# Performance work log

Measured on AMD Instinct MI355X. Metric: run time of the kernel, lower is better.

The kernel has to match this reference:

```python
import jax, jax.numpy as jnp
from jax import lax
import numpy as np

B, T, H, I, O = 256, 2048, 150, 1, 1

def setup_inputs() -> dict:
    key = jax.random.key(0)
    ks = jax.random.split(key, 7)
    s = 1.0 / np.sqrt(H)
    return {
        "input": jax.random.normal(ks[0], (B, T), dtype=jnp.float32),
        "W_ih": jax.random.uniform(ks[1], (3 * H, I), jnp.float32, -s, s),
        "W_hh": jax.random.uniform(ks[2], (3 * H, H), jnp.float32, -s, s),
        "b_ih": jax.random.uniform(ks[3], (3 * H,), jnp.float32, -s, s),
        "b_hh": jax.random.uniform(ks[4], (3 * H,), jnp.float32, -s, s),
        "W_lin": jax.random.uniform(ks[5], (O, H), jnp.float32, -s, s),
        "b_lin": jax.random.uniform(ks[6], (O,), jnp.float32, -s, s),
    }

def reference(input, W_ih, W_hh, b_ih, b_hh, W_lin, b_lin):
    # input: [B, T]; GRUCell recurrence with relu on hidden, per-step linear head.
    hidden = W_hh.shape[1]

    def step(h, x_t):  # h: [B, H], x_t: [B, 1]
        gi = x_t @ W_ih.T + b_ih          # [B, 3H]
        gh = h @ W_hh.T + b_hh            # [B, 3H]
        i_r, i_z, i_n = jnp.split(gi, 3, axis=-1)
        h_r, h_z, h_n = jnp.split(gh, 3, axis=-1)
        r = jax.nn.sigmoid(i_r + h_r)
        z = jax.nn.sigmoid(i_z + h_z)
        n = jnp.tanh(i_n + r * h_n)
        h_new = jax.nn.relu((1.0 - z) * n + z * h)  # relu applied as in original
        y = h_new @ W_lin.T + b_lin       # [B, 1]
        return h_new, y

    xs = jnp.transpose(input)[:, :, None]            # [T, B, 1]
    h0 = jnp.zeros((input.shape[0], hidden), input.dtype)
    _, ys = lax.scan(step, h0, xs)                   # ys: [T, B, 1]
    return jnp.transpose(ys[:, :, 0])                # [B, T] (stack dim=1, squeeze(2))
```

## Files before the change

### kernel.cpp

```cpp
#include <hip/hip_runtime.h>
#include <math.h>


#define BB 256
#define TT 2048
#define HH 150
#define H3 450

typedef float fx2 __attribute__((ext_vector_type(2)));

#define WCLOB \
  "v100","v101","v102","v103","v104","v105","v106","v107","v108","v109", \
  "v110","v111","v112","v113","v114","v115","v116","v117","v118","v119", \
  "v120","v121","v122","v123","v124","v125","v126","v127","v128","v129", \
  "v130","v131","v132","v133","v134","v135","v136","v137","v138","v139", \
  "v140","v141","v142","v143","v144","v145","v146","v147","v148","v149", \
  "v150","v151","v152","v153","v154","v155","v156","v157","v158","v159", \
  "v160","v161","v162","v163","v164","v165","v166","v167","v168","v169", \
  "v170","v171","v172","v173","v174","v175","v176","v177","v178","v179", \
  "v180","v181","v182","v183","v184","v185","v186","v187","v188","v189", \
  "v190","v191","v192","v193","v194","v195","v196","v197","v198","v199", \
  "v200","v201","v202","v203","v204","v205","v206","v207","v208","v209", \
  "v210","v211","v212","v213","v214","v215","v216","v217","v218","v219", \
  "v220","v221","v222","v223","v224","v225","v226","v227","v228","v229", \
  "v230","v231","v232","v233","v234","v235","v236","v237","v238","v239", \
  "v240","v241","v242","v243","v244","v245","v246","v247","v248","v249", \
  "v250","v251"

#define LD4(vA0,vA1,vB0,vB1,OFF) \
  "global_load_dword v" #vA0 ", %[b0], off offset:" #OFF "\n\t" \
  "global_load_dword v" #vA1 ", %[b1], off offset:" #OFF "\n\t" \
  "global_load_dword v" #vB0 ", %[b2], off offset:" #OFF "\n\t" \
  "global_load_dword v" #vB1 ", %[b3], off offset:" #OFF "\n\t"

#define PKB(sp, vp, acc) \
  "v_pk_fma_f32 " acc ", " sp ", " vp ", " acc " op_sel:[0,0,0] op_sel_hi:[0,1,1]\n\t"

#define G4(m0,m1,m2,m3, A0,B0, A1,B1, A2,B2, A3,B3) \
  "v_readlane_b32 s20, %[hq], " #m0 "\n\t" \
  "v_readlane_b32 s22, %[hq], " #m1 "\n\t" \
  "v_readlane_b32 s24, %[hq], " #m2 "\n\t" \
  "v_readlane_b32 s26, %[hq], " #m3 "\n\t" \
  PKB("s[20:21]", A0, "%[a01]") PKB("s[20:21]", B0, "%[a23]") \
  PKB("s[22:23]", A1, "%[a01]") PKB("s[22:23]", B1, "%[a23]") \
  PKB("s[24:25]", A2, "%[a01]") PKB("s[24:25]", B2, "%[a23]") \
  PKB("s[26:27]", A3, "%[a01]") PKB("s[26:27]", B3, "%[a23]")

__global__ __launch_bounds__(512, 2) void gru_seq_kernel(
    const float* __restrict__ input,
    const float* __restrict__ W_ih,
    const float* __restrict__ W_hh,
    const float* __restrict__ b_ih,
    const float* __restrict__ b_hh,
    const float* __restrict__ W_lin,
    const float* __restrict__ b_lin,
    float* __restrict__ out)
{
    const int b    = blockIdx.x;
    const int tid  = threadIdx.x;
    const int lane = tid & 63;
    const int wid  = tid >> 6;
    const int q    = wid & 3;
    const int idx  = ((wid >> 2) << 6) + lane;

    __shared__ float  xrow[TT];
    __shared__ float4 h4[64];
    __shared__ float  PPf[2048];
    __shared__ float  yout[TT];

    ((float4*)xrow)[tid] = ((const float4*)(input + (size_t)b * TT))[tid];
    if (tid < 64) h4[tid] = make_float4(0.f, 0.f, 0.f, 0.f);

    const int r0 = 4 * idx;
#define ROWP(r) ((r) == H3 ? W_lin : W_hh + ((r) < H3 ? (r) : (H3 - 1)) * HH)
    const float* b0 = ROWP(r0)     + q;
    const float* b1 = ROWP(r0 + 1) + q;
    const float* b2 = ROWP(r0 + 2) + q;
    const float* b3 = ROWP(r0 + 3) + q;

    asm volatile(
        LD4(100,101,176,177,0)    LD4(102,103,178,179,16)
        LD4(104,105,180,181,32)   LD4(106,107,182,183,48)
        LD4(108,109,184,185,64)   LD4(110,111,186,187,80)
        LD4(112,113,188,189,96)   LD4(114,115,190,191,112)
        LD4(116,117,192,193,128)  LD4(118,119,194,195,144)
        LD4(120,121,196,197,160)  LD4(122,123,198,199,176)
        LD4(124,125,200,201,192)  LD4(126,127,202,203,208)
        LD4(128,129,204,205,224)  LD4(130,131,206,207,240)
        LD4(132,133,208,209,256)  LD4(134,135,210,211,272)
        LD4(136,137,212,213,288)  LD4(138,139,214,215,304)
        LD4(140,141,216,217,320)  LD4(142,143,218,219,336)
        LD4(144,145,220,221,352)  LD4(146,147,222,223,368)
        LD4(148,149,224,225,384)  LD4(150,151,226,227,400)
        LD4(152,153,228,229,416)  LD4(154,155,230,231,432)
        LD4(156,157,232,233,448)  LD4(158,159,234,235,464)
        LD4(160,161,236,237,480)  LD4(162,163,238,239,496)
        LD4(164,165,240,241,512)  LD4(166,167,242,243,528)
        LD4(168,169,244,245,544)  LD4(170,171,246,247,560)
        LD4(172,173,248,249,576)
        "s_waitcnt vmcnt(0)\n\t"
        :
        : [b0] "v"(b0), [b1] "v"(b1), [b2] "v"(b2), [b3] "v"(b3)
        : WCLOB, "memory");
    {
        const int t37 = (q < 2) ? 148 : 144;
        float w0 = b0[t37], w1 = b1[t37], w2 = b2[t37], w3 = b3[t37];
        asm volatile(
            "v_mov_b32 v174, %0\n\tv_mov_b32 v175, %1\n\t"
            "v_mov_b32 v250, %2\n\tv_mov_b32 v251, %3\n\t"
            :: "v"(w0), "v"(w1), "v"(w2), "v"(w3)
            : "v174","v175","v250","v251");
    }

    float wih_r = 0.f, wih_z = 0.f, wih_n = 0.f;
    float bih_r = 0.f, bih_z = 0.f, bih_n = 0.f;
    float bhh_r = 0.f, bhh_z = 0.f, bhh_n = 0.f;
    if (tid < HH) {
        wih_r = W_ih[tid];          bih_r = b_ih[tid];          bhh_r = b_hh[tid];
        wih_z = W_ih[HH + tid];     bih_z = b_ih[HH + tid];     bhh_z = b_hh[HH + tid];
        wih_n = W_ih[2 * HH + tid]; bih_n = b_ih[2 * HH + tid]; bhh_n = b_hh[2 * HH + tid];
    }
    const float blin = b_lin[0];
    float hreg = 0.f;
    float* outb = out + (size_t)b * TT;
    float2* st01 = (float2*)PPf          + (q << 7) + idx;
    float2* st23 = (float2*)(PPf + 1024) + (q << 7) + idx;
    int ir = 0, iz = 0, in_ = 0;
    if (tid < HH) {
        int r;
        r = tid;        ir  = (((r & 3) >> 1) << 10) + ((r >> 2) << 1) + (r & 1);
        r = HH + tid;   iz  = (((r & 3) >> 1) << 10) + ((r >> 2) << 1) + (r & 1);
        r = 2*HH + tid; in_ = (((r & 3) >> 1) << 10) + ((r >> 2) << 1) + (r & 1);
    }
    const int iy = 1024 + (112 << 1);

    __syncthreads();

    for (int t = 0; t <= TT; ++t) {
        float4 hv = h4[lane];
        float hq = (q == 0) ? hv.x : (q == 1) ? hv.y : (q == 2) ? hv.z : hv.w;
        fx2 a01; a01.x = 0.f; a01.y = 0.f;
        fx2 a23; a23.x = 0.f; a23.y = 0.f;
        asm volatile(
            G4( 0, 1, 2, 3, "v[100:101]","v[176:177]", "v[102:103]","v[178:179]",
                            "v[104:105]","v[180:181]", "v[106:107]","v[182:183]")
            G4( 4, 5, 6, 7, "v[108:109]","v[184:185]", "v[110:111]","v[186:187]",
                            "v[112:113]","v[188:189]", "v[114:115]","v[190:191]")
            G4( 8, 9,10,11, "v[116:117]","v[192:193]", "v[118:119]","v[194:195]",
                            "v[120:121]","v[196:197]", "v[122:123]","v[198:199]")
            G4(12,13,14,15, "v[124:125]","v[200:201]", "v[126:127]","v[202:203]",
                            "v[128:129]","v[204:205]", "v[130:131]","v[206:207]")
            G4(16,17,18,19, "v[132:133]","v[208:209]", "v[134:135]","v[210:211]",
                            "v[136:137]","v[212:213]", "v[138:139]","v[214:215]")
            G4(20,21,22,23, "v[140:141]","v[216:217]", "v[142:143]","v[218:219]",
                            "v[144:145]","v[220:221]", "v[146:147]","v[222:223]")
            G4(24,25,26,27, "v[148:149]","v[224:225]", "v[150:151]","v[226:227]",
                            "v[152:153]","v[228:229]", "v[154:155]","v[230:231]")
            G4(28,29,30,31, "v[156:157]","v[232:233]", "v[158:159]","v[234:235]",
                            "v[160:161]","v[236:237]", "v[162:163]","v[238:239]")
            "v_readlane_b32 s20, %[hq], 32\n\t"
            "v_readlane_b32 s22, %[hq], 33\n\t"
            "v_readlane_b32 s24, %[hq], 34\n\t"
            "v_readlane_b32 s26, %[hq], 35\n\t"
            "v_readlane_b32 s28, %[hq], 36\n\t"
            "v_readlane_b32 s30, %[hq], 37\n\t"
            PKB("s[20:21]", "v[164:165]", "%[a01]")
            PKB("s[20:21]", "v[240:241]", "%[a23]")
            PKB("s[22:23]", "v[166:167]", "%[a01]")
            PKB("s[22:23]", "v[242:243]", "%[a23]")
            PKB("s[24:25]", "v[168:169]", "%[a01]")
            PKB("s[24:25]", "v[244:245]", "%[a23]")
            PKB("s[26:27]", "v[170:171]", "%[a01]")
            PKB("s[26:27]", "v[246:247]", "%[a23]")
            PKB("s[28:29]", "v[172:173]", "%[a01]")
            PKB("s[28:29]", "v[248:249]", "%[a23]")
            PKB("s[30:31]", "v[174:175]", "%[a01]")
            PKB("s[30:31]", "v[250:251]", "%[a23]")
            : [a01] "+v"(a01), [a23] "+v"(a23)
            : [hq] "v"(hq)
            : "s20","s22","s24","s26","s28","s30", WCLOB);
        float2 s0; s0.x = a01.x; s0.y = a01.y;
        float2 s1; s1.x = a23.x; s1.y = a23.y;
        *st01 = s0;
        *st23 = s1;
        __syncthreads();

        if (t < TT && tid < HH) {
            float x  = xrow[t];
            float pr = ((PPf[ir]        + PPf[ir + 256])
                      + (PPf[ir + 512]  + PPf[ir + 768]))  + bhh_r;
            float pz = ((PPf[iz]        + PPf[iz + 256])
                      + (PPf[iz + 512]  + PPf[iz + 768]))  + bhh_z;
            float pn = ((PPf[in_]       + PPf[in_ + 256])
                      + (PPf[in_ + 512] + PPf[in_ + 768])) + bhh_n;
            float gr = fmaf(x, wih_r, bih_r) + pr;
            float gz = fmaf(x, wih_z, bih_z) + pz;
            float r  = 1.f / (1.f + __expf(-gr));
            float z  = 1.f / (1.f + __expf(-gz));
            float ta = fmaf(x, wih_n, bih_n) + r * pn;
            ta = fminf(fmaxf(ta, -15.f), 15.f);
            float e  = __expf(2.f * ta);
            float n  = (e - 1.f) / (e + 1.f);
            float hnew = fmaf(z, hreg - n, n);
            hnew = fmaxf(hnew, 0.f);
            hreg = hnew;
            ((float*)h4)[tid] = hnew;
        }
        if (t > 0 && tid == H3) {
            yout[t - 1] = ((PPf[iy]       + PPf[iy + 256])
                         + (PPf[iy + 512] + PPf[iy + 768])) + blin;
        }
        __syncthreads();
    }

    ((float4*)outb)[tid] = ((const float4*)yout)[tid];
}

extern "C" void kernel_launch(void* const* d_in, const int* in_sizes, int n_in,
                              void* d_out, int out_size, void* d_ws, size_t ws_size,
                              hipStream_t stream) {
    const float* input = (const float*)d_in[0];
    const float* W_ih  = (const float*)d_in[1];
    const float* W_hh  = (const float*)d_in[2];
    const float* b_ih  = (const float*)d_in[3];
    const float* b_hh  = (const float*)d_in[4];
    const float* W_lin = (const float*)d_in[5];
    const float* b_lin = (const float*)d_in[6];
    float* out = (float*)d_out;

    gru_seq_kernel<<<dim3(BB), dim3(512), 0, stream>>>(
        input, W_ih, W_hh, b_ih, b_hh, W_lin, b_lin, out);
}
```

Baseline: 1.834 ms.

## Double-buffer partial sums and keep hidden state in the consuming lanes

Double-buffers the shared partial-sum array so each time step needs only one barrier instead of two. The gate work is remapped so that lane u = 4*lane+q of every wave computes exactly the hidden unit that lane later broadcasts via readlane. This removes the shared h4 round trip, and the unit is computed redundantly in each wave. The output-head reduction is folded into one lane of wave 0. The trade-off is redundant transcendental work in all 8 waves and extra register pressure, with correctness resting on the lane mapping and the parity of the buffers.

```diff
diff --git a/kernel.cpp b/kernel.cpp
--- a/kernel.cpp
+++ b/kernel.cpp
@@ -63,13 +63,11 @@
     const int q    = wid & 3;
     const int idx  = ((wid >> 2) << 6) + lane;
 
-    __shared__ float  xrow[TT];
-    __shared__ float4 h4[64];
-    __shared__ float  PPf[2048];
-    __shared__ float  yout[TT];
+    __shared__ float xrow[TT];
+    __shared__ float PPf[2][2048];
+    __shared__ float yout[TT];
 
     ((float4*)xrow)[tid] = ((const float4*)(input + (size_t)b * TT))[tid];
-    if (tid < 64) h4[tid] = make_float4(0.f, 0.f, 0.f, 0.f);
 
     const int r0 = 4 * idx;
 #define ROWP(r) ((r) == H3 ? W_lin : W_hh + ((r) < H3 ? (r) : (H3 - 1)) * HH)
@@ -112,33 +110,40 @@
             : "v174","v175","v250","v251");
     }
 
+    const int  u       = 4 * lane + q;
+    const bool valid   = (lane < 38) && (u < HH);
+    const bool ywriter = (wid == 0) && (lane == 38);
     float wih_r = 0.f, wih_z = 0.f, wih_n = 0.f;
     float bih_r = 0.f, bih_z = 0.f, bih_n = 0.f;
     float bhh_r = 0.f, bhh_z = 0.f, bhh_n = 0.f;
-    if (tid < HH) {
-        wih_r = W_ih[tid];          bih_r = b_ih[tid];          bhh_r = b_hh[tid];
-        wih_z = W_ih[HH + tid];     bih_z = b_ih[HH + tid];     bhh_z = b_hh[HH + tid];
-        wih_n = W_ih[2 * HH + tid]; bih_n = b_ih[2 * HH + tid]; bhh_n = b_hh[2 * HH + tid];
-    }
-    const float blin = b_lin[0];
-    float hreg = 0.f;
+    if (valid) {
+        wih_r = W_ih[u];          bih_r = b_ih[u];          bhh_r = b_hh[u];
+        wih_z = W_ih[HH + u];     bih_z = b_ih[HH + u];     bhh_z = b_hh[HH + u];
+        wih_n = W_ih[2 * HH + u]; bih_n = b_ih[2 * HH + u]; bhh_n = b_hh[2 * HH + u];
+    }
+    int ir = 0, iz = 0, in_ = 0;
+    if (valid) {
+        int r;
+        r = u;          ir  = (((r & 3) >> 1) << 10) + ((r >> 2) << 1) + (r & 1);
+        r = HH + u;     iz  = (((r & 3) >> 1) << 10) + ((r >> 2) << 1) + (r & 1);
+        r = 2*HH + u;   in_ = (((r & 3) >> 1) << 10) + ((r >> 2) << 1) + (r & 1);
+    }
+    if (ywriter) {
+        ir    = 1024 + (112 << 1);
+        bhh_r = b_lin[0];
+    }
+
+    float hq = 0.f;
     float* outb = out + (size_t)b * TT;
-    float2* st01 = (float2*)PPf          + (q << 7) + idx;
-    float2* st23 = (float2*)(PPf + 1024) + (q << 7) + idx;
-    int ir = 0, iz = 0, in_ = 0;
-    if (tid < HH) {
-        int r;
-        r = tid;        ir  = (((r & 3) >> 1) << 10) + ((r >> 2) << 1) + (r & 1);
-        r = HH + tid;   iz  = (((r & 3) >> 1) << 10) + ((r >> 2) << 1) + (r & 1);
-        r = 2*HH + tid; in_ = (((r & 3) >> 1) << 10) + ((r >> 2) << 1) + (r & 1);
-    }
-    const int iy = 1024 + (112 << 1);
+    float2* st01 = (float2*)PPf + (q << 7) + idx;
+    float2* st23 = (float2*)PPf + 512 + (q << 7) + idx;
 
     __syncthreads();
 
     for (int t = 0; t <= TT; ++t) {
-        float4 hv = h4[lane];
-        float hq = (q == 0) ? hv.x : (q == 1) ? hv.y : (q == 2) ? hv.z : hv.w;
+        const int sel = t & 1;
+        float xt = xrow[t & (TT - 1)];
+
         fx2 a01; a01.x = 0.f; a01.y = 0.f;
         fx2 a23; a23.x = 0.f; a23.y = 0.f;
         asm volatile(
@@ -181,38 +186,36 @@
             : "s20","s22","s24","s26","s28","s30", WCLOB);
         float2 s0; s0.x = a01.x; s0.y = a01.y;
         float2 s1; s1.x = a23.x; s1.y = a23.y;
-        *st01 = s0;
-        *st23 = s1;
+        *(st01 + (sel << 10)) = s0;
+        *(st23 + (sel << 10)) = s1;
         __syncthreads();
 
-        if (t < TT && tid < HH) {
-            float x  = xrow[t];
-            float pr = ((PPf[ir]        + PPf[ir + 256])
-                      + (PPf[ir + 512]  + PPf[ir + 768]))  + bhh_r;
-            float pz = ((PPf[iz]        + PPf[iz + 256])
-                      + (PPf[iz + 512]  + PPf[iz + 768]))  + bhh_z;
-            float pn = ((PPf[in_]       + PPf[in_ + 256])
-                      + (PPf[in_ + 512] + PPf[in_ + 768])) + bhh_n;
-            float gr = fmaf(x, wih_r, bih_r) + pr;
-            float gz = fmaf(x, wih_z, bih_z) + pz;
-            float r  = 1.f / (1.f + __expf(-gr));
-            float z  = 1.f / (1.f + __expf(-gz));
-            float ta = fmaf(x, wih_n, bih_n) + r * pn;
-            ta = fminf(fmaxf(ta, -15.f), 15.f);
-            float e  = __expf(2.f * ta);
-            float n  = (e - 1.f) / (e + 1.f);
-            float hnew = fmaf(z, hreg - n, n);
-            hnew = fmaxf(hnew, 0.f);
-            hreg = hnew;
-            ((float*)h4)[tid] = hnew;
+        const float* pb = &PPf[0][0] + (sel << 11);
+        if ((valid && t < TT) || ywriter) {
+            float pr = ((pb[ir]        + pb[ir + 256])
+                      + (pb[ir + 512]  + pb[ir + 768]))  + bhh_r;
+            if (ywriter) {
+                if (t > 0) yout[t - 1] = pr;
+            } else {
+                float pz = ((pb[iz]        + pb[iz + 256])
+                          + (pb[iz + 512]  + pb[iz + 768]))  + bhh_z;
+                float pn = ((pb[in_]       + pb[in_ + 256])
+                          + (pb[in_ + 512] + pb[in_ + 768])) + bhh_n;
+                float gr = fmaf(xt, wih_r, bih_r) + pr;
+                float gz = fmaf(xt, wih_z, bih_z) + pz;
+                float rr = 1.f / (1.f + __expf(-gr));
+                float zz = 1.f / (1.f + __expf(-gz));
+                float ta = fmaf(xt, wih_n, bih_n) + rr * pn;
+                ta = fminf(fmaxf(ta, -15.f), 15.f);
+                float e  = __expf(2.f * ta);
+                float nn = (e - 1.f) / (e + 1.f);
+                float hnew = fmaf(zz, hq - nn, nn);
+                hq = fmaxf(hnew, 0.f);
+            }
         }
-        if (t > 0 && tid == H3) {
-            yout[t - 1] = ((PPf[iy]       + PPf[iy + 256])
-                         + (PPf[iy + 512] + PPf[iy + 768])) + blin;
-        }
-        __syncthreads();
-    }
-
+    }
+
+    __syncthreads();
     ((float4*)outb)[tid] = ((const float4*)yout)[tid];
 }
 
```

After: 1.991 ms. 1.09x slower.

## Repartition GRU matvec: 8 rows per lane, K split across 8 waves

Applied to the files above, without the earlier changes.

Reorganizes the per-step hidden matvec so each lane owns 8 output rows and each of the 8 waves handles a stride-8 slice of the hidden dimension, replacing 4 rows per lane with a 4-way K split. The goal is to shorten each wave's serial FMA/readlane chain per time step (19 K elements instead of 38), which is the critical path of the recurrence. In exchange, the cross-wave reduction grows from 4 to 8 partial sums per gate, adding LDS reads in the gate-update phase. The LDS layout is padded (stride 65/520) to avoid bank conflicts.

```diff
diff --git a/kernel.cpp b/kernel.cpp
--- a/kernel.cpp
+++ b/kernel.cpp
@@ -27,24 +27,32 @@
   "v240","v241","v242","v243","v244","v245","v246","v247","v248","v249", \
   "v250","v251"
 
-#define LD4(vA0,vA1,vB0,vB1,OFF) \
-  "global_load_dword v" #vA0 ", %[b0], off offset:" #OFF "\n\t" \
-  "global_load_dword v" #vA1 ", %[b1], off offset:" #OFF "\n\t" \
-  "global_load_dword v" #vB0 ", %[b2], off offset:" #OFF "\n\t" \
-  "global_load_dword v" #vB1 ", %[b3], off offset:" #OFF "\n\t"
+#define LD8(a0,a1,b0,b1,c0,c1,d0,d1,OFF) \
+  "global_load_dword v" #a0 ", %[p0], off offset:" #OFF "\n\t" \
+  "global_load_dword v" #a1 ", %[p1], off offset:" #OFF "\n\t" \
+  "global_load_dword v" #b0 ", %[p2], off offset:" #OFF "\n\t" \
+  "global_load_dword v" #b1 ", %[p3], off offset:" #OFF "\n\t" \
+  "global_load_dword v" #c0 ", %[p4], off offset:" #OFF "\n\t" \
+  "global_load_dword v" #c1 ", %[p5], off offset:" #OFF "\n\t" \
+  "global_load_dword v" #d0 ", %[p6], off offset:" #OFF "\n\t" \
+  "global_load_dword v" #d1 ", %[p7], off offset:" #OFF "\n\t"
 
 #define PKB(sp, vp, acc) \
   "v_pk_fma_f32 " acc ", " sp ", " vp ", " acc " op_sel:[0,0,0] op_sel_hi:[0,1,1]\n\t"
 
-#define G4(m0,m1,m2,m3, A0,B0, A1,B1, A2,B2, A3,B3) \
+#define G4(m0,m1,m2,m3, A0,B0,C0,D0, A1,B1,C1,D1, A2,B2,C2,D2, A3,B3,C3,D3) \
   "v_readlane_b32 s20, %[hq], " #m0 "\n\t" \
   "v_readlane_b32 s22, %[hq], " #m1 "\n\t" \
   "v_readlane_b32 s24, %[hq], " #m2 "\n\t" \
   "v_readlane_b32 s26, %[hq], " #m3 "\n\t" \
   PKB("s[20:21]", A0, "%[a01]") PKB("s[20:21]", B0, "%[a23]") \
+  PKB("s[20:21]", C0, "%[a45]") PKB("s[20:21]", D0, "%[a67]") \
   PKB("s[22:23]", A1, "%[a01]") PKB("s[22:23]", B1, "%[a23]") \
+  PKB("s[22:23]", C1, "%[a45]") PKB("s[22:23]", D1, "%[a67]") \
   PKB("s[24:25]", A2, "%[a01]") PKB("s[24:25]", B2, "%[a23]") \
-  PKB("s[26:27]", A3, "%[a01]") PKB("s[26:27]", B3, "%[a23]")
+  PKB("s[24:25]", C2, "%[a45]") PKB("s[24:25]", D2, "%[a67]") \
+  PKB("s[26:27]", A3, "%[a01]") PKB("s[26:27]", B3, "%[a23]") \
+  PKB("s[26:27]", C3, "%[a45]") PKB("s[26:27]", D3, "%[a67]")
 
 __global__ __launch_bounds__(512, 2) void gru_seq_kernel(
     const float* __restrict__ input,
@@ -60,56 +68,63 @@
     const int tid  = threadIdx.x;
     const int lane = tid & 63;
     const int wid  = tid >> 6;
-    const int q    = wid & 3;
-    const int idx  = ((wid >> 2) << 6) + lane;
-
-    __shared__ float  xrow[TT];
-    __shared__ float4 h4[64];
-    __shared__ float  PPf[2048];
-    __shared__ float  yout[TT];
+
+    __shared__ float xrow[TT];
+    __shared__ float PPf[4160];
+    __shared__ float hb[520];
+    __shared__ float yout[TT];
 
     ((float4*)xrow)[tid] = ((const float4*)(input + (size_t)b * TT))[tid];
-    if (tid < 64) h4[tid] = make_float4(0.f, 0.f, 0.f, 0.f);
-
-    const int r0 = 4 * idx;
+    hb[tid < 512 ? tid : 0] = 0.f;
+    if (tid < 8) hb[512 + tid] = 0.f;
+
+    const int r0 = 8 * lane;
 #define ROWP(r) ((r) == H3 ? W_lin : W_hh + ((r) < H3 ? (r) : (H3 - 1)) * HH)
-    const float* b0 = ROWP(r0)     + q;
-    const float* b1 = ROWP(r0 + 1) + q;
-    const float* b2 = ROWP(r0 + 2) + q;
-    const float* b3 = ROWP(r0 + 3) + q;
+    const float* p0 = ROWP(r0)     + wid;
+    const float* p1 = ROWP(r0 + 1) + wid;
+    const float* p2 = ROWP(r0 + 2) + wid;
+    const float* p3 = ROWP(r0 + 3) + wid;
+    const float* p4 = ROWP(r0 + 4) + wid;
+    const float* p5 = ROWP(r0 + 5) + wid;
+    const float* p6 = ROWP(r0 + 6) + wid;
+    const float* p7 = ROWP(r0 + 7) + wid;
 
     asm volatile(
-        LD4(100,101,176,177,0)    LD4(102,103,178,179,16)
-        LD4(104,105,180,181,32)   LD4(106,107,182,183,48)
-        LD4(108,109,184,185,64)   LD4(110,111,186,187,80)
-        LD4(112,113,188,189,96)   LD4(114,115,190,191,112)
-        LD4(116,117,192,193,128)  LD4(118,119,194,195,144)
-        LD4(120,121,196,197,160)  LD4(122,123,198,199,176)
-        LD4(124,125,200,201,192)  LD4(126,127,202,203,208)
-        LD4(128,129,204,205,224)  LD4(130,131,206,207,240)
-        LD4(132,133,208,209,256)  LD4(134,135,210,211,272)
-        LD4(136,137,212,213,288)  LD4(138,139,214,215,304)
-        LD4(140,141,216,217,320)  LD4(142,143,218,219,336)
-        LD4(144,145,220,221,352)  LD4(146,147,222,223,368)
-        LD4(148,149,224,225,384)  LD4(150,151,226,227,400)
-        LD4(152,153,228,229,416)  LD4(154,155,230,231,432)
-        LD4(156,157,232,233,448)  LD4(158,159,234,235,464)
-        LD4(160,161,236,237,480)  LD4(162,163,238,239,496)
-        LD4(164,165,240,241,512)  LD4(166,167,242,243,528)
-        LD4(168,169,244,245,544)  LD4(170,171,246,247,560)
-        LD4(172,173,248,249,576)
+        LD8(100,101,138,139,176,177,214,215, 0)
+        LD8(102,103,140,141,178,179,216,217, 32)
+        LD8(104,105,142,143,180,181,218,219, 64)
+        LD8(106,107,144,145,182,183,220,221, 96)
+        LD8(108,109,146,147,184,185,222,223, 128)
+        LD8(110,111,148,149,186,187,224,225, 160)
+        LD8(112,113,150,151,188,189,226,227, 192)
+        LD8(114,115,152,153,190,191,228,229, 224)
+        LD8(116,117,154,155,192,193,230,231, 256)
+        LD8(118,119,156,157,194,195,232,233, 288)
+        LD8(120,121,158,159,196,197,234,235, 320)
+        LD8(122,123,160,161,198,199,236,237, 352)
+        LD8(124,125,162,163,200,201,238,239, 384)
+        LD8(126,127,164,165,202,203,240,241, 416)
+        LD8(128,129,166,167,204,205,242,243, 448)
+        LD8(130,131,168,169,206,207,244,245, 480)
+        LD8(132,133,170,171,208,209,246,247, 512)
+        LD8(134,135,172,173,210,211,248,249, 544)
         "s_waitcnt vmcnt(0)\n\t"
         :
-        : [b0] "v"(b0), [b1] "v"(b1), [b2] "v"(b2), [b3] "v"(b3)
+        : [p0] "v"(p0), [p1] "v"(p1), [p2] "v"(p2), [p3] "v"(p3),
+          [p4] "v"(p4), [p5] "v"(p5), [p6] "v"(p6), [p7] "v"(p7)
         : WCLOB, "memory");
     {
-        const int t37 = (q < 2) ? 148 : 144;
-        float w0 = b0[t37], w1 = b1[t37], w2 = b2[t37], w3 = b3[t37];
+        const int t18 = (wid < 6) ? 144 : 136;
+        float w0 = p0[t18], w1 = p1[t18], w2 = p2[t18], w3 = p3[t18];
+        float w4 = p4[t18], w5 = p5[t18], w6 = p6[t18], w7 = p7[t18];
         asm volatile(
-            "v_mov_b32 v174, %0\n\tv_mov_b32 v175, %1\n\t"
-            "v_mov_b32 v250, %2\n\tv_mov_b32 v251, %3\n\t"
-            :: "v"(w0), "v"(w1), "v"(w2), "v"(w3)
-            : "v174","v175","v250","v251");
+            "v_mov_b32 v136, %0\n\tv_mov_b32 v137, %1\n\t"
+            "v_mov_b32 v174, %2\n\tv_mov_b32 v175, %3\n\t"
+            "v_mov_b32 v212, %4\n\tv_mov_b32 v213, %5\n\t"
+            "v_mov_b32 v250, %6\n\tv_mov_b32 v251, %7\n\t"
+            :: "v"(w0), "v"(w1), "v"(w2), "v"(w3),
+               "v"(w4), "v"(w5), "v"(w6), "v"(w7)
+            : "v136","v137","v174","v175","v212","v213","v250","v251");
     }
 
     float wih_r = 0.f, wih_z = 0.f, wih_n = 0.f;
@@ -123,76 +138,88 @@
     const float blin = b_lin[0];
     float hreg = 0.f;
     float* outb = out + (size_t)b * TT;
-    float2* st01 = (float2*)PPf          + (q << 7) + idx;
-    float2* st23 = (float2*)(PPf + 1024) + (q << 7) + idx;
+    float2* st = (float2*)PPf + wid * 260 + lane;
     int ir = 0, iz = 0, in_ = 0;
     if (tid < HH) {
         int r;
-        r = tid;        ir  = (((r & 3) >> 1) << 10) + ((r >> 2) << 1) + (r & 1);
-        r = HH + tid;   iz  = (((r & 3) >> 1) << 10) + ((r >> 2) << 1) + (r & 1);
-        r = 2*HH + tid; in_ = (((r & 3) >> 1) << 10) + ((r >> 2) << 1) + (r & 1);
-    }
-    const int iy = 1024 + (112 << 1);
+        r = tid;        ir  = (((r & 7) >> 1) * 65 + (r >> 3)) * 2 + (r & 1);
+        r = HH + tid;   iz  = (((r & 7) >> 1) * 65 + (r >> 3)) * 2 + (r & 1);
+        r = 2*HH + tid; in_ = (((r & 7) >> 1) * 65 + (r >> 3)) * 2 + (r & 1);
+    }
+    const int iy = (1 * 65 + 56) * 2;
 
     __syncthreads();
 
     for (int t = 0; t <= TT; ++t) {
-        float4 hv = h4[lane];
-        float hq = (q == 0) ? hv.x : (q == 1) ? hv.y : (q == 2) ? hv.z : hv.w;
+        float hq = hb[wid * 65 + lane];
         fx2 a01; a01.x = 0.f; a01.y = 0.f;
         fx2 a23; a23.x = 0.f; a23.y = 0.f;
+        fx2 a45; a45.x = 0.f; a45.y = 0.f;
+        fx2 a67; a67.x = 0.f; a67.y = 0.f;
         asm volatile(
-            G4( 0, 1, 2, 3, "v[100:101]","v[176:177]", "v[102:103]","v[178:179]",
-                            "v[104:105]","v[180:181]", "v[106:107]","v[182:183]")
-            G4( 4, 5, 6, 7, "v[108:109]","v[184:185]", "v[110:111]","v[186:187]",
-                            "v[112:113]","v[188:189]", "v[114:115]","v[190:191]")
-            G4( 8, 9,10,11, "v[116:117]","v[192:193]", "v[118:119]","v[194:195]",
-                            "v[120:121]","v[196:197]", "v[122:123]","v[198:199]")
-            G4(12,13,14,15, "v[124:125]","v[200:201]", "v[126:127]","v[202:203]",
-                            "v[128:129]","v[204:205]", "v[130:131]","v[206:207]")
-            G4(16,17,18,19, "v[132:133]","v[208:209]", "v[134:135]","v[210:211]",
-                            "v[136:137]","v[212:213]", "v[138:139]","v[214:215]")
-            G4(20,21,22,23, "v[140:141]","v[216:217]", "v[142:143]","v[218:219]",
-                            "v[144:145]","v[220:221]", "v[146:147]","v[222:223]")
-            G4(24,25,26,27, "v[148:149]","v[224:225]", "v[150:151]","v[226:227]",
-                            "v[152:153]","v[228:229]", "v[154:155]","v[230:231]")
-            G4(28,29,30,31, "v[156:157]","v[232:233]", "v[158:159]","v[234:235]",
-                            "v[160:161]","v[236:237]", "v[162:163]","v[238:239]")
-            "v_readlane_b32 s20, %[hq], 32\n\t"
-            "v_readlane_b32 s22, %[hq], 33\n\t"
-            "v_readlane_b32 s24, %[hq], 34\n\t"
-            "v_readlane_b32 s26, %[hq], 35\n\t"
-            "v_readlane_b32 s28, %[hq], 36\n\t"
-            "v_readlane_b32 s30, %[hq], 37\n\t"
-            PKB("s[20:21]", "v[164:165]", "%[a01]")
-            PKB("s[20:21]", "v[240:241]", "%[a23]")
-            PKB("s[22:23]", "v[166:167]", "%[a01]")
-            PKB("s[22:23]", "v[242:243]", "%[a23]")
-            PKB("s[24:25]", "v[168:169]", "%[a01]")
-            PKB("s[24:25]", "v[244:245]", "%[a23]")
-            PKB("s[26:27]", "v[170:171]", "%[a01]")
-            PKB("s[26:27]", "v[246:247]", "%[a23]")
-            PKB("s[28:29]", "v[172:173]", "%[a01]")
-            PKB("s[28:29]", "v[248:249]", "%[a23]")
-            PKB("s[30:31]", "v[174:175]", "%[a01]")
-            PKB("s[30:31]", "v[250:251]", "%[a23]")
-            : [a01] "+v"(a01), [a23] "+v"(a23)
+            G4( 0, 1, 2, 3,
+                "v[100:101]","v[138:139]","v[176:177]","v[214:215]",
+                "v[102:103]","v[140:141]","v[178:179]","v[216:217]",
+                "v[104:105]","v[142:143]","v[180:181]","v[218:219]",
+                "v[106:107]","v[144:145]","v[182:183]","v[220:221]")
+            G4( 4, 5, 6, 7,
+                "v[108:109]","v[146:147]","v[184:185]","v[222:223]",
+                "v[110:111]","v[148:149]","v[186:187]","v[224:225]",
+                "v[112:113]","v[150:151]","v[188:189]","v[226:227]",
+                "v[114:115]","v[152:153]","v[190:191]","v[228:229]")
+            G4( 8, 9,10,11,
+                "v[116:117]","v[154:155]","v[192:193]","v[230:231]",
+                "v[118:119]","v[156:157]","v[194:195]","v[232:233]",
+                "v[120:121]","v[158:159]","v[196:197]","v[234:235]",
+                "v[122:123]","v[160:161]","v[198:199]","v[236:237]")
+            G4(12,13,14,15,
+                "v[124:125]","v[162:163]","v[200:201]","v[238:239]",
+                "v[126:127]","v[164:165]","v[202:203]","v[240:241]",
+                "v[128:129]","v[166:167]","v[204:205]","v[242:243]",
+                "v[130:131]","v[168:169]","v[206:207]","v[244:245]")
+            "v_readlane_b32 s28, %[hq], 16\n\t"
+            "v_readlane_b32 s30, %[hq], 17\n\t"
+            "v_readlane_b32 s20, %[hq], 18\n\t"
+            PKB("s[28:29]", "v[132:133]", "%[a01]")
+            PKB("s[28:29]", "v[170:171]", "%[a23]")
+            PKB("s[28:29]", "v[208:209]", "%[a45]")
+            PKB("s[28:29]", "v[246:247]", "%[a67]")
+            PKB("s[30:31]", "v[134:135]", "%[a01]")
+            PKB("s[30:31]", "v[172:173]", "%[a23]")
+            PKB("s[30:31]", "v[210:211]", "%[a45]")
+            PKB("s[30:31]", "v[248:249]", "%[a67]")
+            PKB("s[20:21]", "v[136:137]", "%[a01]")
+            PKB("s[20:21]", "v[174:175]", "%[a23]")
+            PKB("s[20:21]", "v[212:213]", "%[a45]")
+            PKB("s[20:21]", "v[250:251]", "%[a67]")
+            : [a01] "+v"(a01), [a23] "+v"(a23),
+              [a45] "+v"(a45), [a67] "+v"(a67)
             : [hq] "v"(hq)
             : "s20","s22","s24","s26","s28","s30", WCLOB);
-        float2 s0; s0.x = a01.x; s0.y = a01.y;
-        float2 s1; s1.x = a23.x; s1.y = a23.y;
-        *st01 = s0;
-        *st23 = s1;
+        float2 s01; s01.x = a01.x; s01.y = a01.y;
+        float2 s23; s23.x = a23.x; s23.y = a23.y;
+        float2 s45; s45.x = a45.x; s45.y = a45.y;
+        float2 s67; s67.x = a67.x; s67.y = a67.y;
+        st[0]   = s01;
+        st[65]  = s23;
+        st[130] = s45;
+        st[195] = s67;
         __syncthreads();
 
         if (t < TT && tid < HH) {
             float x  = xrow[t];
-            float pr = ((PPf[ir]        + PPf[ir + 256])
-                      + (PPf[ir + 512]  + PPf[ir + 768]))  + bhh_r;
-            float pz = ((PPf[iz]        + PPf[iz + 256])
-                      + (PPf[iz + 512]  + PPf[iz + 768]))  + bhh_z;
-            float pn = ((PPf[in_]       + PPf[in_ + 256])
-                      + (PPf[in_ + 512] + PPf[in_ + 768])) + bhh_n;
+            float pr = (((PPf[ir]         + PPf[ir + 520])
+                       + (PPf[ir + 1040]  + PPf[ir + 1560]))
+                      + ((PPf[ir + 2080]  + PPf[ir + 2600])
+                       + (PPf[ir + 3120]  + PPf[ir + 3640]))) + bhh_r;
+            float pz = (((PPf[iz]         + PPf[iz + 520])
+                       + (PPf[iz + 1040]  + PPf[iz + 1560]))
+                      + ((PPf[iz + 2080]  + PPf[iz + 2600])
+                       + (PPf[iz + 3120]  + PPf[iz + 3640]))) + bhh_z;
+            float pn = (((PPf[in_]        + PPf[in_ + 520])
+                       + (PPf[in_ + 1040] + PPf[in_ + 1560]))
+                      + ((PPf[in_ + 2080] + PPf[in_ + 2600])
+                       + (PPf[in_ + 3120] + PPf[in_ + 3640]))) + bhh_n;
             float gr = fmaf(x, wih_r, bih_r) + pr;
             float gz = fmaf(x, wih_z, bih_z) + pz;
             float r  = 1.f / (1.f + __expf(-gr));
@@ -204,11 +231,13 @@
             float hnew = fmaf(z, hreg - n, n);
             hnew = fmaxf(hnew, 0.f);
             hreg = hnew;
-            ((float*)h4)[tid] = hnew;
+            hb[(tid & 7) * 65 + (tid >> 3)] = hnew;
         }
         if (t > 0 && tid == H3) {
-            yout[t - 1] = ((PPf[iy]       + PPf[iy + 256])
-                         + (PPf[iy + 512] + PPf[iy + 768])) + blin;
+            yout[t - 1] = (((PPf[iy]        + PPf[iy + 520])
+                          + (PPf[iy + 1040] + PPf[iy + 1560]))
+                         + ((PPf[iy + 2080] + PPf[iy + 2600])
+                          + (PPf[iy + 3120] + PPf[iy + 3640]))) + blin;
         }
         __syncthreads();
     }
```

Result: slower. 1.881 ms (+2.6%).

## Broadcast hidden state via LDS reads instead of readlane, pad partial-sum buffer

Applied to the files above, without the earlier changes.

Replaces the per-step v_readlane scalar broadcast of the hidden vector with ds_read_b64 loads from a transposed shared hidden buffer, feeding packed FMAs through op_sel halves and pipelining the LDS reads against compute with staged waitcnts. The partial-sum buffer is padded (strides 130/260/520) to reduce bank conflicts, and the divisions in sigmoid/tanh become hardware reciprocal approximations. The goal is to remove the serial readlane/SGPR dependency chain and bank conflicts in the recurrence's critical path. It risks LDS latency exposure and slightly less accurate activations.

```diff
diff --git a/kernel.cpp b/kernel.cpp
--- a/kernel.cpp
+++ b/kernel.cpp
@@ -27,24 +27,26 @@
   "v240","v241","v242","v243","v244","v245","v246","v247","v248","v249", \
   "v250","v251"
 
+#define HCLOB \
+  "v80","v81","v82","v83","v84","v85","v86","v87","v88","v89", \
+  "v90","v91","v92","v93","v94","v95","v96","v97","v98","v99"
+
 #define LD4(vA0,vA1,vB0,vB1,OFF) \
   "global_load_dword v" #vA0 ", %[b0], off offset:" #OFF "\n\t" \
   "global_load_dword v" #vA1 ", %[b1], off offset:" #OFF "\n\t" \
   "global_load_dword v" #vB0 ", %[b2], off offset:" #OFF "\n\t" \
   "global_load_dword v" #vB1 ", %[b3], off offset:" #OFF "\n\t"
 
-#define PKB(sp, vp, acc) \
-  "v_pk_fma_f32 " acc ", " sp ", " vp ", " acc " op_sel:[0,0,0] op_sel_hi:[0,1,1]\n\t"
-
-#define G4(m0,m1,m2,m3, A0,B0, A1,B1, A2,B2, A3,B3) \
-  "v_readlane_b32 s20, %[hq], " #m0 "\n\t" \
-  "v_readlane_b32 s22, %[hq], " #m1 "\n\t" \
-  "v_readlane_b32 s24, %[hq], " #m2 "\n\t" \
-  "v_readlane_b32 s26, %[hq], " #m3 "\n\t" \
-  PKB("s[20:21]", A0, "%[a01]") PKB("s[20:21]", B0, "%[a23]") \
-  PKB("s[22:23]", A1, "%[a01]") PKB("s[22:23]", B1, "%[a23]") \
-  PKB("s[24:25]", A2, "%[a01]") PKB("s[24:25]", B2, "%[a23]") \
-  PKB("s[26:27]", A3, "%[a01]") PKB("s[26:27]", B3, "%[a23]")
+#define PKBL(hp, wp, acc) \
+  "v_pk_fma_f32 " acc ", " hp ", " wp ", " acc " op_sel:[0,0,0] op_sel_hi:[0,1,1]\n\t"
+#define PKBH(hp, wp, acc) \
+  "v_pk_fma_f32 " acc ", " hp ", " wp ", " acc " op_sel:[1,0,0] op_sel_hi:[1,1,1]\n\t"
+#define PKML(hp, wp, acc) \
+  "v_pk_mul_f32 " acc ", " hp ", " wp " op_sel:[0,0] op_sel_hi:[0,1]\n\t"
+
+#define C0(P, A, B)  PKML(P, A, "%[a01]") PKML(P, B, "%[a23]")
+#define CPL(P, A, B) PKBL(P, A, "%[a01]") PKBL(P, B, "%[a23]")
+#define CPH(P, A, B) PKBH(P, A, "%[a01]") PKBH(P, B, "%[a23]")
 
 __global__ __launch_bounds__(512, 2) void gru_seq_kernel(
     const float* __restrict__ input,
@@ -63,13 +65,13 @@
     const int q    = wid & 3;
     const int idx  = ((wid >> 2) << 6) + lane;
 
-    __shared__ float  xrow[TT];
-    __shared__ float4 h4[64];
-    __shared__ float  PPf[2048];
-    __shared__ float  yout[TT];
+    __shared__ float xrow[TT];
+    __shared__ float PPf[2080];
+    __shared__ __align__(16) float hb[160];
+    __shared__ float yout[TT];
 
     ((float4*)xrow)[tid] = ((const float4*)(input + (size_t)b * TT))[tid];
-    if (tid < 64) h4[tid] = make_float4(0.f, 0.f, 0.f, 0.f);
+    if (tid < 160) hb[tid] = 0.f;
 
     const int r0 = 4 * idx;
 #define ROWP(r) ((r) == H3 ? W_lin : W_hh + ((r) < H3 ? (r) : (H3 - 1)) * HH)
@@ -123,92 +125,122 @@
     const float blin = b_lin[0];
     float hreg = 0.f;
     float* outb = out + (size_t)b * TT;
-    float2* st01 = (float2*)PPf          + (q << 7) + idx;
-    float2* st23 = (float2*)(PPf + 1024) + (q << 7) + idx;
+    float2* st = (float2*)PPf + q * 130 + idx;
+    const unsigned hva = (unsigned)(size_t)(&hb[q * 40]);
     int ir = 0, iz = 0, in_ = 0;
     if (tid < HH) {
         int r;
-        r = tid;        ir  = (((r & 3) >> 1) << 10) + ((r >> 2) << 1) + (r & 1);
-        r = HH + tid;   iz  = (((r & 3) >> 1) << 10) + ((r >> 2) << 1) + (r & 1);
-        r = 2*HH + tid; in_ = (((r & 3) >> 1) << 10) + ((r >> 2) << 1) + (r & 1);
-    }
-    const int iy = 1024 + (112 << 1);
+        r = tid;        ir  = ((r & 3) >> 1) * 1040 + ((r >> 2) << 1) + (r & 1);
+        r = HH + tid;   iz  = ((r & 3) >> 1) * 1040 + ((r >> 2) << 1) + (r & 1);
+        r = 2*HH + tid; in_ = ((r & 3) >> 1) * 1040 + ((r >> 2) << 1) + (r & 1);
+    }
+    const int iy = 1040 + 112 * 2;
 
     __syncthreads();
 
     for (int t = 0; t <= TT; ++t) {
-        float4 hv = h4[lane];
-        float hq = (q == 0) ? hv.x : (q == 1) ? hv.y : (q == 2) ? hv.z : hv.w;
-        fx2 a01; a01.x = 0.f; a01.y = 0.f;
-        fx2 a23; a23.x = 0.f; a23.y = 0.f;
+        fx2 a01, a23;
         asm volatile(
-            G4( 0, 1, 2, 3, "v[100:101]","v[176:177]", "v[102:103]","v[178:179]",
-                            "v[104:105]","v[180:181]", "v[106:107]","v[182:183]")
-            G4( 4, 5, 6, 7, "v[108:109]","v[184:185]", "v[110:111]","v[186:187]",
-                            "v[112:113]","v[188:189]", "v[114:115]","v[190:191]")
-            G4( 8, 9,10,11, "v[116:117]","v[192:193]", "v[118:119]","v[194:195]",
-                            "v[120:121]","v[196:197]", "v[122:123]","v[198:199]")
-            G4(12,13,14,15, "v[124:125]","v[200:201]", "v[126:127]","v[202:203]",
-                            "v[128:129]","v[204:205]", "v[130:131]","v[206:207]")
-            G4(16,17,18,19, "v[132:133]","v[208:209]", "v[134:135]","v[210:211]",
-                            "v[136:137]","v[212:213]", "v[138:139]","v[214:215]")
-            G4(20,21,22,23, "v[140:141]","v[216:217]", "v[142:143]","v[218:219]",
-                            "v[144:145]","v[220:221]", "v[146:147]","v[222:223]")
-            G4(24,25,26,27, "v[148:149]","v[224:225]", "v[150:151]","v[226:227]",
-                            "v[152:153]","v[228:229]", "v[154:155]","v[230:231]")
-            G4(28,29,30,31, "v[156:157]","v[232:233]", "v[158:159]","v[234:235]",
-                            "v[160:161]","v[236:237]", "v[162:163]","v[238:239]")
-            "v_readlane_b32 s20, %[hq], 32\n\t"
-            "v_readlane_b32 s22, %[hq], 33\n\t"
-            "v_readlane_b32 s24, %[hq], 34\n\t"
-            "v_readlane_b32 s26, %[hq], 35\n\t"
-            "v_readlane_b32 s28, %[hq], 36\n\t"
-            "v_readlane_b32 s30, %[hq], 37\n\t"
-            PKB("s[20:21]", "v[164:165]", "%[a01]")
-            PKB("s[20:21]", "v[240:241]", "%[a23]")
-            PKB("s[22:23]", "v[166:167]", "%[a01]")
-            PKB("s[22:23]", "v[242:243]", "%[a23]")
-            PKB("s[24:25]", "v[168:169]", "%[a01]")
-            PKB("s[24:25]", "v[244:245]", "%[a23]")
-            PKB("s[26:27]", "v[170:171]", "%[a01]")
-            PKB("s[26:27]", "v[246:247]", "%[a23]")
-            PKB("s[28:29]", "v[172:173]", "%[a01]")
-            PKB("s[28:29]", "v[248:249]", "%[a23]")
-            PKB("s[30:31]", "v[174:175]", "%[a01]")
-            PKB("s[30:31]", "v[250:251]", "%[a23]")
-            : [a01] "+v"(a01), [a23] "+v"(a23)
-            : [hq] "v"(hq)
-            : "s20","s22","s24","s26","s28","s30", WCLOB);
-        float2 s0; s0.x = a01.x; s0.y = a01.y;
-        float2 s1; s1.x = a23.x; s1.y = a23.y;
-        *st01 = s0;
-        *st23 = s1;
+            "ds_read_b64 v[80:81], %[va] offset:0\n\t"
+            "ds_read_b64 v[82:83], %[va] offset:8\n\t"
+            "ds_read_b64 v[84:85], %[va] offset:16\n\t"
+            "ds_read_b64 v[86:87], %[va] offset:24\n\t"
+            "ds_read_b64 v[88:89], %[va] offset:32\n\t"
+            "ds_read_b64 v[90:91], %[va] offset:40\n\t"
+            "ds_read_b64 v[92:93], %[va] offset:48\n\t"
+            "ds_read_b64 v[94:95], %[va] offset:56\n\t"
+            "ds_read_b64 v[96:97], %[va] offset:64\n\t"
+            "ds_read_b64 v[98:99], %[va] offset:72\n\t"
+            "s_waitcnt lgkmcnt(8)\n\t"
+            C0 ("v[80:81]", "v[100:101]", "v[176:177]")
+            CPH("v[80:81]", "v[102:103]", "v[178:179]")
+            CPL("v[82:83]", "v[104:105]", "v[180:181]")
+            CPH("v[82:83]", "v[106:107]", "v[182:183]")
+            "s_waitcnt lgkmcnt(6)\n\t"
+            CPL("v[84:85]", "v[108:109]", "v[184:185]")
+            CPH("v[84:85]", "v[110:111]", "v[186:187]")
+            CPL("v[86:87]", "v[112:113]", "v[188:189]")
+            CPH("v[86:87]", "v[114:115]", "v[190:191]")
+            "ds_read_b64 v[80:81], %[va] offset:80\n\t"
+            "ds_read_b64 v[82:83], %[va] offset:88\n\t"
+            "ds_read_b64 v[84:85], %[va] offset:96\n\t"
+            "ds_read_b64 v[86:87], %[va] offset:104\n\t"
+            "s_waitcnt lgkmcnt(8)\n\t"
+            CPL("v[88:89]", "v[116:117]", "v[192:193]")
+            CPH("v[88:89]", "v[118:119]", "v[194:195]")
+            CPL("v[90:91]", "v[120:121]", "v[196:197]")
+            CPH("v[90:91]", "v[122:123]", "v[198:199]")
+            "s_waitcnt lgkmcnt(6)\n\t"
+            CPL("v[92:93]", "v[124:125]", "v[200:201]")
+            CPH("v[92:93]", "v[126:127]", "v[202:203]")
+            CPL("v[94:95]", "v[128:129]", "v[204:205]")
+            CPH("v[94:95]", "v[130:131]", "v[206:207]")
+            "ds_read_b64 v[88:89], %[va] offset:112\n\t"
+            "ds_read_b64 v[90:91], %[va] offset:120\n\t"
+            "ds_read_b64 v[92:93], %[va] offset:128\n\t"
+            "ds_read_b64 v[94:95], %[va] offset:136\n\t"
+            "s_waitcnt lgkmcnt(8)\n\t"
+            CPL("v[96:97]", "v[132:133]", "v[208:209]")
+            CPH("v[96:97]", "v[134:135]", "v[210:211]")
+            CPL("v[98:99]", "v[136:137]", "v[212:213]")
+            CPH("v[98:99]", "v[138:139]", "v[214:215]")
+            "ds_read_b64 v[96:97], %[va] offset:144\n\t"
+            "s_waitcnt lgkmcnt(7)\n\t"
+            CPL("v[80:81]", "v[140:141]", "v[216:217]")
+            CPH("v[80:81]", "v[142:143]", "v[218:219]")
+            CPL("v[82:83]", "v[144:145]", "v[220:221]")
+            CPH("v[82:83]", "v[146:147]", "v[222:223]")
+            "s_waitcnt lgkmcnt(5)\n\t"
+            CPL("v[84:85]", "v[148:149]", "v[224:225]")
+            CPH("v[84:85]", "v[150:151]", "v[226:227]")
+            CPL("v[86:87]", "v[152:153]", "v[228:229]")
+            CPH("v[86:87]", "v[154:155]", "v[230:231]")
+            "s_waitcnt lgkmcnt(3)\n\t"
+            CPL("v[88:89]", "v[156:157]", "v[232:233]")
+            CPH("v[88:89]", "v[158:159]", "v[234:235]")
+            CPL("v[90:91]", "v[160:161]", "v[236:237]")
+            CPH("v[90:91]", "v[162:163]", "v[238:239]")
+            "s_waitcnt lgkmcnt(1)\n\t"
+            CPL("v[92:93]", "v[164:165]", "v[240:241]")
+            CPH("v[92:93]", "v[166:167]", "v[242:243]")
+            CPL("v[94:95]", "v[168:169]", "v[244:245]")
+            CPH("v[94:95]", "v[170:171]", "v[246:247]")
+            "s_waitcnt lgkmcnt(0)\n\t"
+            CPL("v[96:97]", "v[172:173]", "v[248:249]")
+            CPH("v[96:97]", "v[174:175]", "v[250:251]")
+            : [a01] "=&v"(a01), [a23] "=&v"(a23)
+            : [va] "v"(hva)
+            : HCLOB, WCLOB);
+        float2 s01; s01.x = a01.x; s01.y = a01.y;
+        float2 s23; s23.x = a23.x; s23.y = a23.y;
+        st[0]   = s01;
+        st[520] = s23;
         __syncthreads();
 
         if (t < TT && tid < HH) {
             float x  = xrow[t];
-            float pr = ((PPf[ir]        + PPf[ir + 256])
-                      + (PPf[ir + 512]  + PPf[ir + 768]))  + bhh_r;
-            float pz = ((PPf[iz]        + PPf[iz + 256])
-                      + (PPf[iz + 512]  + PPf[iz + 768]))  + bhh_z;
-            float pn = ((PPf[in_]       + PPf[in_ + 256])
-                      + (PPf[in_ + 512] + PPf[in_ + 768])) + bhh_n;
+            float pr = ((PPf[ir]        + PPf[ir + 260])
+                      + (PPf[ir + 520]  + PPf[ir + 780]))  + bhh_r;
+            float pz = ((PPf[iz]        + PPf[iz + 260])
+                      + (PPf[iz + 520]  + PPf[iz + 780]))  + bhh_z;
+            float pn = ((PPf[in_]       + PPf[in_ + 260])
+                      + (PPf[in_ + 520] + PPf[in_ + 780])) + bhh_n;
             float gr = fmaf(x, wih_r, bih_r) + pr;
             float gz = fmaf(x, wih_z, bih_z) + pz;
-            float r  = 1.f / (1.f + __expf(-gr));
-            float z  = 1.f / (1.f + __expf(-gz));
+            float r  = __builtin_amdgcn_rcpf(1.f + __expf(-gr));
+            float z  = __builtin_amdgcn_rcpf(1.f + __expf(-gz));
             float ta = fmaf(x, wih_n, bih_n) + r * pn;
             ta = fminf(fmaxf(ta, -15.f), 15.f);
             float e  = __expf(2.f * ta);
-            float n  = (e - 1.f) / (e + 1.f);
+            float n  = (e - 1.f) * __builtin_amdgcn_rcpf(e + 1.f);
             float hnew = fmaf(z, hreg - n, n);
             hnew = fmaxf(hnew, 0.f);
             hreg = hnew;
-            ((float*)h4)[tid] = hnew;
+            hb[(tid & 3) * 40 + (tid >> 2)] = hnew;
         }
         if (t > 0 && tid == H3) {
-            yout[t - 1] = ((PPf[iy]       + PPf[iy + 256])
-                         + (PPf[iy + 512] + PPf[iy + 768])) + blin;
+            yout[t - 1] = ((PPf[iy]       + PPf[iy + 260])
+                         + (PPf[iy + 520] + PPf[iy + 780])) + blin;
         }
         __syncthreads();
     }
```

After: 1.600 ms. 1.15x faster.
